# Kernel tuning notes

Measured on AMD Instinct MI355X. Metric: run time of the kernel, lower is better.

Reference implementation:

```python
import jax, jax.numpy as jnp
from jax import lax
import numpy as np

B, T, D, H, C = 128, 256, 512, 1024, 512

def _kaiming(key, shape):
    fan_in = shape[1]
    return jax.random.normal(key, shape, dtype=jnp.float32) * np.sqrt(2.0 / fan_in)

def setup_inputs() -> dict:
    key = jax.random.key(0)
    ks = jax.random.split(key, 9)
    x = jax.random.randint(ks[0], (B, T), 0, D)
    embed = jax.random.normal(ks[1], (D, D), dtype=jnp.float32)  # nn.Embedding default N(0,1)
    return {
        "x": x,
        "embed": embed,
        "W_z": _kaiming(ks[2], (H, D)),
        "U_z": _kaiming(ks[3], (H, H)),
        "W_r": _kaiming(ks[4], (H, D)),
        "U_r": _kaiming(ks[5], (H, H)),
        "W": _kaiming(ks[6], (H, D)),
        "U": _kaiming(ks[7], (H, H)),
        "W_ph": _kaiming(ks[8], (C, H)),
        "b_p": jnp.zeros((C, 1), dtype=jnp.float32),
    }

def reference(x, embed, W_z, U_z, W_r, U_r, W, U, W_ph, b_p):
    x_emb = embed[x]  # [B, T, D]
    # Precompute all input-side gate projections, time-major [T, H, B]
    Wx_z = jnp.einsum('hd,btd->thb', W_z, x_emb)
    Wx_r = jnp.einsum('hd,btd->thb', W_r, x_emb)
    Wx_h = jnp.einsum('hd,btd->thb', W, x_emb)

    def step(h, gates):
        wxz, wxr, wxh = gates
        z = jax.nn.sigmoid(wxz + U_z @ h)
        r = jax.nn.sigmoid(wxr + U_r @ h)
        h_hat = jnp.tanh(wxh + r * (U @ h))
        h_new = jnp.tanh(z * h + (1.0 - z) * h_hat)  # note: outer tanh as in source
        return h_new, None

    h0 = jnp.zeros((W_z.shape[0], x.shape[0]), dtype=x_emb.dtype)  # [H, B]
    h_t, _ = lax.scan(step, h0, (Wx_z, Wx_r, Wx_h))
    y = W_ph @ h_t + b_p  # [C, B]
    y = jax.nn.log_softmax(y, axis=0)
    return y.T  # [B, C]
```

## Files before the change

### kernel.cpp

```cpp
#include <hip/hip_runtime.h>
#include <hip/hip_bf16.h>

#define B_ 128
#define T_ 256
#define DV 512
#define H_ 1024
#define C_ 512

typedef _Float16 half8 __attribute__((ext_vector_type(8)));
typedef _Float16 half4 __attribute__((ext_vector_type(4)));
typedef float f32x4 __attribute__((ext_vector_type(4)));
typedef unsigned long long ull;
typedef unsigned long long ull2 __attribute__((ext_vector_type(2)));

#define SENT 0x7C007C007C007C00ULL

__device__ __forceinline__ float sigmoidf_(float x){ return 1.f/(1.f+__expf(-x)); }
__device__ __forceinline__ float tanhf_(float x){
  x = fminf(12.f, fmaxf(-12.f, x));
  float e = __expf(2.f*x);
  return (e-1.f)/(e+1.f);
}
__device__ __forceinline__ f32x4 mfma16(half8 a, half8 b, f32x4 c){
  return __builtin_amdgcn_mfma_f32_16x16x32_f16(a, b, c, 0, 0, 0);
}
__device__ __forceinline__ bool ok8(ull v){
  return ((unsigned)v & 0xFFFFu) != 0x7C00u;
}
#define LDA(p) __hip_atomic_load((p), __ATOMIC_RELAXED, __HIP_MEMORY_SCOPE_AGENT)


__global__ void k_transpose_x(const int* __restrict__ x, int* __restrict__ xT){
  int idx = blockIdx.x*256 + threadIdx.x;
  int t = idx >> 7, b = idx & 127;
  xT[idx] = x[b*T_ + t];
}

__global__ __launch_bounds__(256) void k_compute_PT16(
    const float* __restrict__ embed,
    const float* __restrict__ Wz, const float* __restrict__ Wr, const float* __restrict__ Wh,
    float* __restrict__ PT){
  const int tid = threadIdx.x, lane = tid & 63, w = tid >> 6;
  const int wid = blockIdx.x*4 + w;
  const int g   = wid >> 11;
  const int rem = wid & 2047;
  const int ht  = rem >> 5;
  const int tt  = rem & 31;
  const float* Wg = (g==0)?Wz:((g==1)?Wr:Wh);

  const int hrow = ht*16 + (lane & 15);
  const int tcol = tt*16 + (lane & 15);
  const int kb   = 4*(lane >> 4);
  const float* arow = Wg    + (size_t)hrow*DV;
  const float* brow = embed + (size_t)tcol*DV;

  f32x4 acc = {0,0,0,0};
  #pragma unroll 4
  for (int kc=0; kc<16; ++kc){
    f32x4 alo = *(const f32x4*)(arow + kc*32 + kb);
    f32x4 ahi = *(const f32x4*)(arow + kc*32 + 16 + kb);
    f32x4 blo = *(const f32x4*)(brow + kc*32 + kb);
    f32x4 bhi = *(const f32x4*)(brow + kc*32 + 16 + kb);
    half8 a, b;
    #pragma unroll
    for (int e=0; e<4; ++e){
      a[e] = (_Float16)alo[e]; a[e+4] = (_Float16)ahi[e];
      b[e] = (_Float16)blo[e]; b[e+4] = (_Float16)bhi[e];
    }
    acc = mfma16(a, b, acc);
  }
  float* P = PT + (size_t)g*DV*H_;
  *(f32x4*)(P + (size_t)tcol*H_ + ht*16 + 4*(lane>>4)) = acc;
}

__global__ __launch_bounds__(256) void k_build_Ufrag(
    const float* __restrict__ Uz, const float* __restrict__ Ur, const float* __restrict__ Uh,
    half8* __restrict__ Ufrag){
  int idx = blockIdx.x*256 + threadIdx.x;
  int l  = idx & 63;
  int kc = (idx>>6) & 31;
  int rt = (idx>>11) & 63;
  int g  = idx>>17;
  const float* Ug = (g==0)?Uz:((g==1)?Ur:Uh);
  int row = rt*16 + (l&15);
  int kb  = kc*32 + 4*(l>>4);
  f32x4 lo = *(const f32x4*)(Ug + (size_t)row*H_ + kb);
  f32x4 hi = *(const f32x4*)(Ug + (size_t)row*H_ + kb + 16);
  half8 o;
  o[0]=(_Float16)lo[0]; o[1]=(_Float16)lo[1]; o[2]=(_Float16)lo[2]; o[3]=(_Float16)lo[3];
  o[4]=(_Float16)hi[0]; o[5]=(_Float16)hi[1]; o[6]=(_Float16)hi[2]; o[7]=(_Float16)hi[3];
  Ufrag[idx] = o;
}

__global__ void k_fill_sentinel(ull* __restrict__ p){
  p[blockIdx.x*256 + threadIdx.x] = SENT;
}

__global__ __launch_bounds__(256, 1) void k_gru_persist(
    const half8* __restrict__ Ufrag,
    const float* __restrict__ PT,
    const int* __restrict__ xT,
    half8* __restrict__ hbuf0,
    half8* __restrict__ hbuf1,
    half8* __restrict__ hbuf2)
{
  __shared__ half8 hs[2][2048];

  const int tid = threadIdx.x, lane = tid & 63, w = tid >> 6;
  const int wg  = blockIdx.x;
  const int c   = wg & 7;
  const int rb  = wg >> 3;
  const int rt  = rb*4 + w;
  const int kh  = rt >> 1;

  half8 u0[32], u1[32], u2[32];
  #pragma unroll
  for (int j=0; j<32; ++j) u0[j] = Ufrag[(((0*64+rt)*32) + j)*64 + lane];
  #pragma unroll
  for (int j=0; j<32; ++j) u1[j] = Ufrag[(((1*64+rt)*32) + j)*64 + lane];
  #pragma unroll
  for (int j=0; j<32; ++j) u2[j] = Ufrag[(((2*64+rt)*32) + j)*64 + lane];

  const int col = c*16 + (lane & 15);
  const int q = lane >> 4;
  const int rowq = rt*16 + 4*q;
  const float* PTz = PT;
  const float* PTr = PT + (size_t)DV*H_;
  const float* PTh = PT + (size_t)2*DV*H_;

  const half8* pa = hbuf0;
  const half8* pb = hbuf1;
  const half8* pc = hbuf2;

  for (int t=0; t<T_; ++t){
    const int par = t & 1;

    int token = xT[t*B_ + col];
    f32x4 pz = *(const f32x4*)(PTz + (size_t)token*H_ + rowq);
    f32x4 pr = *(const f32x4*)(PTr + (size_t)token*H_ + rowq);
    f32x4 ph = *(const f32x4*)(PTh + (size_t)token*H_ + rowq);

    const ull* sbase = (const ull*)pa + (((size_t)((tid>>6)*8 + c)*64 + (tid&63)) << 1);
    ull va[16];
    unsigned miss = 0xFFu;
    #pragma unroll
    for (int s=0; s<8; ++s){
      va[2*s]   = LDA(sbase + s*4096);
      va[2*s+1] = LDA(sbase + s*4096 + 1);
    }
    #pragma unroll
    for (int s=0; s<8; ++s)
      if (ok8(va[2*s]) && ok8(va[2*s+1])) miss &= ~(1u<<s);
    int guard = 0;
    while (miss && ++guard < (1<<13)){
      __builtin_amdgcn_s_sleep(4);
      #pragma unroll
      for (int s=0; s<8; ++s){
        if (miss & (1u<<s)){
          va[2*s]   = LDA(sbase + s*4096);
          va[2*s+1] = LDA(sbase + s*4096 + 1);
        }
      }
      #pragma unroll
      for (int s=0; s<8; ++s){
        if ((miss & (1u<<s)) && ok8(va[2*s]) && ok8(va[2*s+1])) miss &= ~(1u<<s);
      }
    }
    #pragma unroll
    for (int s=0; s<8; ++s){
      ull2 wv; wv[0] = va[2*s]; wv[1] = va[2*s+1];
      hs[par][tid + s*256] = __builtin_bit_cast(half8, wv);
    }
    __syncthreads();

    size_t slot = (((size_t)(kh*8 + c)*64 + lane) << 1) | (unsigned)(rt & 1);
    __hip_atomic_store((ull*)pc + slot, SENT, __ATOMIC_RELAXED, __HIP_MEMORY_SCOPE_AGENT);

    f32x4 az={0,0,0,0}, ar={0,0,0,0}, ah={0,0,0,0};
    #pragma unroll
    for (int j=0; j<32; ++j){
      half8 b = hs[par][j*64 + lane];
      az = mfma16(u0[j], b, az);
      ar = mfma16(u1[j], b, ar);
      ah = mfma16(u2[j], b, ah);
    }
    half4 hold = ((half4*)hs[par])[((kh*64 + lane) << 1) | (rt & 1)];

    half4 ho;
    #pragma unroll
    for (int r=0; r<4; ++r){
      float z  = sigmoidf_(pz[r] + az[r]);
      float rr = sigmoidf_(pr[r] + ar[r]);
      float hh = tanhf_(ph[r] + rr*ah[r]);
      float hp = (float)hold[r];
      float hn = tanhf_(z*hp + (1.f-z)*hh);
      ho[r] = (_Float16)hn;
    }
    ull hval = __builtin_bit_cast(ull, ho);
    asm volatile("s_waitcnt vmcnt(0)" ::: "memory");
    __hip_atomic_store((ull*)pb + slot, hval, __ATOMIC_RELAXED, __HIP_MEMORY_SCOPE_AGENT);

    const half8* tmp = pa; pa = pb; pb = pc; pc = tmp;
  }
}


__global__ __launch_bounds__(256) void k_out_gemm(
    const _Float16* __restrict__ hf, const float* __restrict__ Wph,
    const float* __restrict__ bp, float* __restrict__ yT){
  __shared__ float hsm[64][128];
  int tid = threadIdx.x;
  int c0 = blockIdx.x*16;
  int cl = tid>>4, bg = tid&15;
  float acc[8] = {0,0,0,0,0,0,0,0};
  for(int i0=0;i0<H_;i0+=64){
    __syncthreads();
    for(int i=tid;i<64*128;i+=256){
      int r=i>>7, b=i&127;
      int ih = i0 + r;
      int kc = ih>>5, kr = ih&31;
      int l  = ((kr>>2)&3)*16 + (b&15);
      int e  = (kr>>4)*4 + (kr&3);
      int ct = b>>4;
      hsm[r][b] = (float)hf[(((kc*8+ct)*64 + l)<<3) + e];
    }
    __syncthreads();
    for(int il=0; il<64; ++il){
      float wv = Wph[(size_t)(c0+cl)*H_ + i0 + il];
      const float* hrow = &hsm[il][bg*8];
      #pragma unroll
      for(int j=0;j<8;++j) acc[j] += wv * hrow[j];
    }
  }
  float bias = bp[c0+cl];
  #pragma unroll
  for(int j=0;j<8;++j){
    int b = bg*8+j;
    yT[(size_t)b*C_ + c0+cl] = acc[j] + bias;
  }
}

__global__ __launch_bounds__(256) void k_logsoftmax(const float* __restrict__ yT, float* __restrict__ out){
  __shared__ float red[256];
  int b = blockIdx.x, tid = threadIdx.x;
  float v0 = yT[(size_t)b*C_ + tid];
  float v1 = yT[(size_t)b*C_ + 256 + tid];
  red[tid] = fmaxf(v0,v1); __syncthreads();
  for(int s=128;s>0;s>>=1){ if(tid<s) red[tid]=fmaxf(red[tid],red[tid+s]); __syncthreads(); }
  float M = red[0]; __syncthreads();
  red[tid] = __expf(v0-M)+__expf(v1-M); __syncthreads();
  for(int s=128;s>0;s>>=1){ if(tid<s) red[tid]+=red[tid+s]; __syncthreads(); }
  float L = M + logf(red[0]);
  out[(size_t)b*C_ + tid]       = v0 - L;
  out[(size_t)b*C_ + 256 + tid] = v1 - L;
}


extern "C" void kernel_launch(void* const* d_in, const int* in_sizes, int n_in,
                              void* d_out, int out_size, void* d_ws, size_t ws_size,
                              hipStream_t stream){
  const int*   x    = (const int*)  d_in[0];
  const float* embed= (const float*)d_in[1];
  const float* Wz   = (const float*)d_in[2];
  const float* Uz   = (const float*)d_in[3];
  const float* Wr   = (const float*)d_in[4];
  const float* Ur   = (const float*)d_in[5];
  const float* Wh   = (const float*)d_in[6];
  const float* Uh   = (const float*)d_in[7];
  const float* Wph  = (const float*)d_in[8];
  const float* bp   = (const float*)d_in[9];
  float* out = (float*)d_out;

  char* w = (char*)d_ws;
  float*    PT    = (float*)(w);
  half8*    Ufrag = (half8*)(w + (6u<<20));
  _Float16* hbuf0 = (_Float16*)(w + (12u<<20));
  _Float16* hbuf1 = (_Float16*)(w + (12u<<20) + (256u<<10));
  _Float16* hbuf2 = (_Float16*)(w + (12u<<20) + (512u<<10));
  int*      xT    = (int*)(w + (12u<<20) + (768u<<10));
  float*    yT    = (float*)(w + (12u<<20) + (896u<<10));

  k_transpose_x<<<128,256,0,stream>>>(x, xT);
  k_compute_PT16<<<1536,256,0,stream>>>(embed, Wz, Wr, Wh, PT);
  k_build_Ufrag<<<1536,256,0,stream>>>(Uz, Ur, Uh, Ufrag);
  (void)hipMemsetAsync(hbuf0, 0, 256u<<10, stream);
  k_fill_sentinel<<<128,256,0,stream>>>((ull*)hbuf1);
  k_fill_sentinel<<<128,256,0,stream>>>((ull*)hbuf2);

  k_gru_persist<<<dim3(128), dim3(256), 0, stream>>>(
      (const half8*)Ufrag, PT, xT,
      (half8*)hbuf0, (half8*)hbuf1, (half8*)hbuf2);

  k_out_gemm<<<32,256,0,stream>>>(hbuf1, Wph, bp, yT);
  k_logsoftmax<<<128,256,0,stream>>>(yT, out);
}
```

Baseline: 1.165 ms.

## Add XCD-aware fast path for same-die h exchange via L2 atomics

```diff
diff --git a/kernel.cpp b/kernel.cpp
--- a/kernel.cpp
+++ b/kernel.cpp
@@ -28,6 +28,30 @@
   return ((unsigned)v & 0xFFFFu) != 0x7C00u;
 }
 #define LDA(p) __hip_atomic_load((p), __ATOMIC_RELAXED, __HIP_MEMORY_SCOPE_AGENT)
+#define STA(p,v) __hip_atomic_store((p), (v), __ATOMIC_RELAXED, __HIP_MEMORY_SCOPE_AGENT)
+
+__device__ __forceinline__ void atom8_l2(ull* p, ull v[8]){
+  ull z = 0;
+  ull *a0=p,       *a1=p+1,     *a2=p+4096,  *a3=p+4097,
+      *a4=p+8192,  *a5=p+8193,  *a6=p+12288, *a7=p+12289;
+  asm volatile(
+    "global_atomic_or_x2 %0, %8,  %16, off sc0\n\t"
+    "global_atomic_or_x2 %1, %9,  %16, off sc0\n\t"
+    "global_atomic_or_x2 %2, %10, %16, off sc0\n\t"
+    "global_atomic_or_x2 %3, %11, %16, off sc0\n\t"
+    "global_atomic_or_x2 %4, %12, %16, off sc0\n\t"
+    "global_atomic_or_x2 %5, %13, %16, off sc0\n\t"
+    "global_atomic_or_x2 %6, %14, %16, off sc0\n\t"
+    "global_atomic_or_x2 %7, %15, %16, off sc0\n\t"
+    "s_waitcnt vmcnt(0)"
+    : "=&v"(v[0]),"=&v"(v[1]),"=&v"(v[2]),"=&v"(v[3]),
+      "=&v"(v[4]),"=&v"(v[5]),"=&v"(v[6]),"=&v"(v[7])
+    : "v"(a0),"v"(a1),"v"(a2),"v"(a3),"v"(a4),"v"(a5),"v"(a6),"v"(a7),"v"(z)
+    : "memory");
+}
+__device__ __forceinline__ void st_swap_l2(ull* p, ull v){
+  asm volatile("global_atomic_swap_x2 %0, %1, off" :: "v"(p), "v"(v) : "memory");
+}
 
 
 __global__ void k_transpose_x(const int* __restrict__ x, int* __restrict__ xT){
@@ -100,11 +124,13 @@
     const half8* __restrict__ Ufrag,
     const float* __restrict__ PT,
     const int* __restrict__ xT,
-    half8* __restrict__ hbuf0,
-    half8* __restrict__ hbuf1,
-    half8* __restrict__ hbuf2)
+    half8* __restrict__ hbuf0, half8* __restrict__ hbuf1, half8* __restrict__ hbuf2,
+    half8* __restrict__ hfa0,  half8* __restrict__ hfa1,  half8* __restrict__ hfa2,
+    unsigned* __restrict__ xcdtab)
 {
   __shared__ half8 hs[2][2048];
+  __shared__ unsigned s_tab[128];
+  __shared__ unsigned s_sane;
 
   const int tid = threadIdx.x, lane = tid & 63, w = tid >> 6;
   const int wg  = blockIdx.x;
@@ -112,6 +138,38 @@
   const int rb  = wg >> 3;
   const int rt  = rb*4 + w;
   const int kh  = rt >> 1;
+
+  unsigned myxcd;
+  asm volatile("s_getreg_b32 %0, hwreg(HW_REG_XCC_ID, 0, 32)" : "=s"(myxcd));
+  myxcd &= 0xFFu;
+  if (tid == 0) STA(&xcdtab[wg], myxcd | 0x100u);
+  if (tid < 128){
+    unsigned v = 0; int g1 = 0;
+    do { v = LDA(&xcdtab[tid]); } while (!(v & 0x100u) && ++g1 < (1<<14));
+    s_tab[tid] = v;
+  }
+  __syncthreads();
+  if (tid == 0){
+    unsigned cnt[8] = {0,0,0,0,0,0,0,0};
+    bool all = true;
+    for (int i=0;i<128;i++){
+      unsigned v = s_tab[i];
+      if (!(v & 0x100u) || (v & 0xFFu) > 7u){ all = false; break; }
+      cnt[v & 7u]++;
+    }
+    unsigned distinct=0, maxg=0;
+    if (all) for (int x=0;x<8;x++){ if(cnt[x]){ distinct++; if(cnt[x]>maxg) maxg=cnt[x]; } }
+    s_sane = (all && distinct >= 2u && maxg <= 64u) ? 1u : 0u;
+  }
+  __syncthreads();
+  unsigned fastmask = 0;
+  if (s_sane && myxcd < 8u){
+    #pragma unroll
+    for (int s=0; s<8; ++s){
+      int wgp = (2*s + (w>>1))*8 + c;
+      if ((s_tab[wgp] & 0xFFu) == myxcd) fastmask |= (1u<<s);
+    }
+  }
 
   half8 u0[32], u1[32], u2[32];
   #pragma unroll
@@ -128,9 +186,10 @@
   const float* PTr = PT + (size_t)DV*H_;
   const float* PTh = PT + (size_t)2*DV*H_;
 
-  const half8* pa = hbuf0;
-  const half8* pb = hbuf1;
-  const half8* pc = hbuf2;
+  const half8* pa = hbuf0; const half8* pb = hbuf1; const half8* pc = hbuf2;
+  half8* fa = hfa0; half8* fb = hfa1; half8* fc = hfa2;
+
+  const size_t toff = (((size_t)((tid>>6)*8 + c)*64 + (tid&63)) << 1);
 
   for (int t=0; t<T_; ++t){
     const int par = t & 1;
@@ -140,30 +199,60 @@
     f32x4 pr = *(const f32x4*)(PTr + (size_t)token*H_ + rowq);
     f32x4 ph = *(const f32x4*)(PTh + (size_t)token*H_ + rowq);
 
-    const ull* sbase = (const ull*)pa + (((size_t)((tid>>6)*8 + c)*64 + (tid&63)) << 1);
+    const ull* sbase = (const ull*)pa + toff;
+    ull*       fbT   = (ull*)fa + toff;
     ull va[16];
     unsigned miss = 0xFFu;
-    #pragma unroll
-    for (int s=0; s<8; ++s){
-      va[2*s]   = LDA(sbase + s*4096);
-      va[2*s+1] = LDA(sbase + s*4096 + 1);
-    }
-    #pragma unroll
-    for (int s=0; s<8; ++s)
-      if (ok8(va[2*s]) && ok8(va[2*s+1])) miss &= ~(1u<<s);
-    int guard = 0;
-    while (miss && ++guard < (1<<13)){
-      __builtin_amdgcn_s_sleep(4);
+
+    if (fastmask){
+      ull fv[16];
+      atom8_l2(fbT,         fv);
+      atom8_l2(fbT + 16384, fv + 8);
       #pragma unroll
-      for (int s=0; s<8; ++s){
-        if (miss & (1u<<s)){
+      for (int s=0; s<8; ++s)
+        if (((fastmask>>s)&1u) && ok8(fv[2*s]) && ok8(fv[2*s+1])){
+          va[2*s] = fv[2*s]; va[2*s+1] = fv[2*s+1];
+          miss &= ~(1u<<s);
+        }
+    }
+    {
+      unsigned mm = miss & ~fastmask;
+      if (mm){
+        #pragma unroll
+        for (int s=0; s<8; ++s) if ((mm>>s)&1u){
           va[2*s]   = LDA(sbase + s*4096);
           va[2*s+1] = LDA(sbase + s*4096 + 1);
         }
+        #pragma unroll
+        for (int s=0; s<8; ++s)
+          if (((mm>>s)&1u) && ok8(va[2*s]) && ok8(va[2*s+1])) miss &= ~(1u<<s);
       }
-      #pragma unroll
-      for (int s=0; s<8; ++s){
-        if ((miss & (1u<<s)) && ok8(va[2*s]) && ok8(va[2*s+1])) miss &= ~(1u<<s);
+    }
+    int guard = 0;
+    while (miss && ++guard < (1<<13)){
+      unsigned fm = miss & fastmask;
+      unsigned mm = (guard > 48) ? miss : (miss & ~fastmask);
+      if (fm){
+        ull fv[16];
+        atom8_l2(fbT,         fv);
+        atom8_l2(fbT + 16384, fv + 8);
+        #pragma unroll
+        for (int s=0; s<8; ++s)
+          if (((fm>>s)&1u) && ok8(fv[2*s]) && ok8(fv[2*s+1])){
+            va[2*s] = fv[2*s]; va[2*s+1] = fv[2*s+1];
+            miss &= ~(1u<<s);
+          }
+      }
+      if (mm){
+        __builtin_amdgcn_s_sleep(4);
+        #pragma unroll
+        for (int s=0; s<8; ++s) if ((mm>>s)&1u){
+          va[2*s]   = LDA(sbase + s*4096);
+          va[2*s+1] = LDA(sbase + s*4096 + 1);
+        }
+        #pragma unroll
+        for (int s=0; s<8; ++s)
+          if (((mm>>s)&1u) && ok8(va[2*s]) && ok8(va[2*s+1])) miss &= ~(1u<<s);
       }
     }
     #pragma unroll
@@ -174,7 +263,8 @@
     __syncthreads();
 
     size_t slot = (((size_t)(kh*8 + c)*64 + lane) << 1) | (unsigned)(rt & 1);
-    __hip_atomic_store((ull*)pc + slot, SENT, __ATOMIC_RELAXED, __HIP_MEMORY_SCOPE_AGENT);
+    st_swap_l2((ull*)fc + slot, SENT);
+    STA((ull*)pc + slot, SENT);
 
     f32x4 az={0,0,0,0}, ar={0,0,0,0}, ah={0,0,0,0};
     #pragma unroll
@@ -197,10 +287,13 @@
       ho[r] = (_Float16)hn;
     }
     ull hval = __builtin_bit_cast(ull, ho);
-    asm volatile("s_waitcnt vmcnt(0)" ::: "memory");
-    __hip_atomic_store((ull*)pb + slot, hval, __ATOMIC_RELAXED, __HIP_MEMORY_SCOPE_AGENT);
-
-    const half8* tmp = pa; pa = pb; pb = pc; pc = tmp;
+    asm volatile("s_waitcnt vmcnt(1)" ::: "memory");
+    st_swap_l2((ull*)fb + slot, hval);
+    asm volatile("s_waitcnt vmcnt(1)" ::: "memory");
+    STA((ull*)pb + slot, hval);
+
+    const half8* tm = pa; pa = pb; pb = pc; pc = tm;
+    half8* tf = fa; fa = fb; fb = fc; fc = tf;
   }
 }
 
@@ -279,17 +372,27 @@
   _Float16* hbuf2 = (_Float16*)(w + (12u<<20) + (512u<<10));
   int*      xT    = (int*)(w + (12u<<20) + (768u<<10));
   float*    yT    = (float*)(w + (12u<<20) + (896u<<10));
+  _Float16* hfa0  = (_Float16*)(w + (12u<<20) + (1152u<<10));
+  _Float16* hfa1  = (_Float16*)(w + (12u<<20) + (1408u<<10));
+  _Float16* hfa2  = (_Float16*)(w + (12u<<20) + (1664u<<10));
+  unsigned* xcdtab= (unsigned*)(w + (12u<<20) + (1920u<<10));
 
   k_transpose_x<<<128,256,0,stream>>>(x, xT);
   k_compute_PT16<<<1536,256,0,stream>>>(embed, Wz, Wr, Wh, PT);
   k_build_Ufrag<<<1536,256,0,stream>>>(Uz, Ur, Uh, Ufrag);
   (void)hipMemsetAsync(hbuf0, 0, 256u<<10, stream);
+  (void)hipMemsetAsync(hfa0,  0, 256u<<10, stream);
+  (void)hipMemsetAsync(xcdtab, 0, 512, stream);
   k_fill_sentinel<<<128,256,0,stream>>>((ull*)hbuf1);
   k_fill_sentinel<<<128,256,0,stream>>>((ull*)hbuf2);
+  k_fill_sentinel<<<128,256,0,stream>>>((ull*)hfa1);
+  k_fill_sentinel<<<128,256,0,stream>>>((ull*)hfa2);
 
   k_gru_persist<<<dim3(128), dim3(256), 0, stream>>>(
       (const half8*)Ufrag, PT, xT,
-      (half8*)hbuf0, (half8*)hbuf1, (half8*)hbuf2);
+      (half8*)hbuf0, (half8*)hbuf1, (half8*)hbuf2,
+      (half8*)hfa0,  (half8*)hfa1,  (half8*)hfa2,
+      xcdtab);
 
   k_out_gemm<<<32,256,0,stream>>>(hbuf1, Wph, bp, yT);
   k_logsoftmax<<<128,256,0,stream>>>(yT, out);
```

New measurement: 3.864 ms. 3.32x slower.
